# Optimization experiments

Hardware: AMD Instinct MI355X
Metric: run time of the kernel (lower is better)

## Reference

```python
import jax, jax.numpy as jnp
import numpy as np

B, CIN, D, H, W = 2, 64, 64, 64, 64
NUM_CLASSES = 5
STRIDE = 2
NMAX = 32
TOPK = 13
TAL_ALPHA, TAL_BETA = 1.0, 6.0
EPS = 1e-9


def setup_inputs() -> dict:
    key = jax.random.key(0)
    ks = jax.random.split(key, 6)
    features = jax.random.normal(ks[0], (B, CIN, D, H, W), jnp.float32)
    cls_w = jax.random.normal(ks[1], (NUM_CLASSES, CIN, 3, 3, 3), jnp.float32) * 0.02
    cls_b = jnp.zeros((NUM_CLASSES,), jnp.float32)
    off_w = jax.random.normal(ks[2], (3, CIN, 3, 3, 3), jnp.float32) * 0.01
    off_b = jnp.zeros((3,), jnp.float32)
    coords = jax.random.uniform(ks[3], (B, NMAX, 3), jnp.float32, 4.0, float(D * STRIDE) - 4.0)
    cls = jax.random.randint(ks[4], (B, NMAX, 1), 0, NUM_CLASSES).astype(jnp.float32)
    sigma = jax.random.uniform(ks[5], (B, NMAX, 1), jnp.float32, 2.0, 8.0)
    pad = (jnp.arange(NMAX) >= 24)[None, :, None]  # last 8 GT slots are padding
    cls = jnp.where(pad, -100.0, cls)
    labels = jnp.concatenate([coords, cls, sigma], axis=-1)  # B N 5 : x,y,z,class,sigma
    return {"features": features, "cls_w": cls_w, "cls_b": cls_b,
            "off_w": off_w, "off_b": off_b, "labels": labels}


def conv3d(x, w, b):
    y = jax.lax.conv_general_dilated(x, w, (1, 1, 1), 'SAME',
                                     dimension_numbers=('NCDHW', 'OIDHW', 'NCDHW'))
    return y + b[None, :, None, None, None]


def make_anchors():
    g = jnp.stack(jnp.meshgrid(jnp.arange(D), jnp.arange(H), jnp.arange(W), indexing='ij'))
    return (g.astype(jnp.float32) + 0.5) * STRIDE  # (3, D, H, W)


def flatten_bchw(x):
    # B C D H W -> B (D H W) C
    Bsz, C = x.shape[0], x.shape[1]
    return x.transpose(0, 2, 3, 4, 1).reshape(Bsz, -1, C)


def tal_assign(pred_logits, pred_centers, true_labels, true_centers, true_sigmas, valid):
    # pred_logits (B,L,C); pred_centers (B,L,3); true_* (B,N,...); valid (B,N) bool
    Bsz, L, C = pred_logits.shape
    N = true_labels.shape[1]
    d2 = jnp.sum((true_centers[:, :, None, :] - pred_centers[:, None, :, :]) ** 2, -1)  # B N L
    ious = jnp.exp(-d2 / (2.0 * true_sigmas[:, :, None] ** 2))  # keypoint IoU, B N L
    probs = jax.nn.sigmoid(pred_logits).transpose(0, 2, 1)  # B C L
    cls_scores = jnp.take_along_axis(probs, true_labels[:, :, None], axis=1)  # B N L
    align = (cls_scores ** TAL_ALPHA) * (ious ** TAL_BETA)  # alignment metric
    topv, topi = jax.lax.top_k(align, TOPK)
    is_topk = jnp.zeros_like(align).at[
        jnp.arange(Bsz)[:, None, None], jnp.arange(N)[None, :, None], topi
    ].set(jnp.where(topv > EPS, 1.0, 0.0))
    mask_pos = is_topk * valid[:, :, None].astype(align.dtype)  # B N L
    pos_sum = mask_pos.sum(axis=1)  # B L
    # resolve anchors matched to multiple GTs: keep GT with max IoU
    is_max_iou = jax.nn.one_hot(jnp.argmax(ious, axis=1), N, axis=1, dtype=align.dtype)
    mask_pos = jnp.where(pos_sum[:, None, :] > 1, is_max_iou, mask_pos)
    pos_sum = mask_pos.sum(axis=1)
    fg = pos_sum > 0  # B L
    assigned_gt = jnp.argmax(mask_pos, axis=1)  # B L
    assigned_labels = jnp.take_along_axis(true_labels, assigned_gt, axis=1)
    assigned_labels = jnp.where(fg, assigned_labels, C)  # bg_index = C
    assigned_centers = jnp.take_along_axis(true_centers, assigned_gt[:, :, None], axis=1)  # B L 3
    assigned_sigmas = jnp.take_along_axis(true_sigmas, assigned_gt, axis=1)  # B L
    align = align * mask_pos
    max_align = align.max(axis=2, keepdims=True)  # B N 1
    max_iou = (ious * mask_pos).max(axis=2, keepdims=True)
    score = (align * max_iou / (max_align + EPS)).max(axis=1)  # B L
    assigned_scores = jax.nn.one_hot(assigned_labels, C + 1)[..., :C] * score[..., None]  # B L C
    return assigned_labels, assigned_centers, assigned_scores, assigned_sigmas


def detection_loss(logits, offsets, anchors, labels):
    pred_logits = flatten_bchw(logits)               # B L C
    pred_centers = flatten_bchw(anchors + offsets)   # B L 3
    anchor_pts = flatten_bchw(anchors)
    C = pred_logits.shape[-1]
    true_centers = labels[..., :3]
    true_labels_f = labels[..., 3]
    true_sigmas = labels[..., 4]
    valid = true_labels_f != -100.0
    true_labels = jnp.where(valid, true_labels_f, 0.0).astype(jnp.int32)
    assigned = tal_assign(jax.lax.stop_gradient(pred_logits),
                          jax.lax.stop_gradient(pred_centers),
                          true_labels, true_centers, true_sigmas, valid)
    assigned_labels, assigned_centers, assigned_scores, assigned_sigmas = jax.lax.stop_gradient(assigned)
    one_hot_label = jax.nn.one_hot(assigned_labels, C + 1)[..., :C]
    # varifocal loss (alpha=0.75, gamma=2)
    p = jax.nn.sigmoid(pred_logits)
    weight = 0.75 * (p ** 2.0) * (1.0 - one_hot_label) + assigned_scores * one_hot_label
    bce = assigned_scores * jax.nn.softplus(-pred_logits) + (1.0 - assigned_scores) * jax.nn.softplus(pred_logits)
    cls_loss = jnp.sum(weight * bce)
    d = jnp.sum((pred_centers - assigned_centers) ** 2, -1)  # B L
    w = assigned_scores.sum(-1)
    iou = jnp.exp(-d / (2.0 * assigned_sigmas ** 2))
    mask_positive = assigned_labels != C
    reg_loss = jnp.sum(jnp.where(mask_positive, (1.0 - iou) * w, 0.0))
    return (cls_loss + reg_loss) / assigned_scores.sum()


def reference(features, cls_w, cls_b, off_w, off_b, labels):
    logits = conv3d(features, cls_w, cls_b)    # B C D H W
    offsets = conv3d(features, off_w, off_b)   # B 3 D H W
    anchors = jnp.broadcast_to(make_anchors()[None], (features.shape[0], 3, D, H, W))
    loss = detection_loss(logits, offsets, anchors, labels)
    return loss
```

## Files before the change

### kernel.cpp

```cpp
#include <hip/hip_runtime.h>
#include <math.h>

#define NB 2
#define CIN 64
#define DD_ 64
#define HH_ 64
#define WW_ 64
#define NCLS 5
#define LL (DD_*HH_*WW_)
#define NMAXG 32
#define TOPKK 13
#define NSLAB 4
#define BUFSZ 38016

typedef __attribute__((ext_vector_type(16))) float floatx16;

__device__ __forceinline__ float softplusf_(float z){
  return fmaxf(z, 0.f) + log1pf(expf(-fabsf(z)));
}
__device__ __forceinline__ float sigmoidf_(float z){
  return 1.f/(1.f + expf(-z));
}
__device__ __forceinline__ unsigned tofp8_(float x){
  unsigned u = __float_as_uint(x);
  unsigned sign = (u >> 24) & 0x80u;
  unsigned a = u & 0x7FFFFFFFu;
  if (a >= 0x43E00000u) return sign | 0x7Eu;
  if (a < 0x3C800000u){
    float fa = __uint_as_float(a);
    int m = (int)rintf(fa * 512.f);
    return sign | (unsigned)m;
  }
  unsigned bb = a + 0x7FFFFu + ((a >> 20) & 1u);
  unsigned e8 = ((bb >> 23) & 0xFFu) - 120u;
  unsigned m8 = (bb >> 20) & 7u;
  if (e8 > 15u || (e8 == 15u && m8 > 6u)) return sign | 0x7Eu;
  return sign | (e8 << 3) | m8;
}

__global__ __launch_bounds__(256) void transpose_kernel(
    const float* __restrict__ feat, unsigned char* __restrict__ featT,
    const float* __restrict__ cls_w, const float* __restrict__ off_w,
    unsigned char* __restrict__ wA, float* __restrict__ bgz)
{
  const int t = threadIdx.x;
  const int w = t & 63;
  const int hh = t >> 6;
  const int d = blockIdx.x;
  const int h = blockIdx.y*4 + hh;
  const int b = blockIdx.z;
  const float* src = feat + (size_t)b*CIN*LL + (size_t)d*4096 + (size_t)h*64 + w;
  const size_t sp = (size_t)d*4096 + (size_t)h*64 + w;
  #pragma unroll
  for (int cc=0; cc<4; ++cc){
    unsigned q[16];
    #pragma unroll
    for (int j=0;j<16;++j) q[j] = tofp8_(src[(size_t)(cc*16+j)*LL]);
    uint4 p;
    p.x = q[0] | (q[1]<<8) | (q[2]<<16) | (q[3]<<24);
    p.y = q[4] | (q[5]<<8) | (q[6]<<16) | (q[7]<<24);
    p.z = q[8] | (q[9]<<8) | (q[10]<<16) | (q[11]<<24);
    p.w = q[12] | (q[13]<<8) | (q[14]<<16) | (q[15]<<24);
    *(uint4*)(featT + ((size_t)(b*4+cc)*LL + sp)*16) = p;
  }
  if (blockIdx.z == 0 && blockIdx.y == 0 && blockIdx.x < 54){
    if (blockIdx.x == 0 && t < 2) bgz[t] = 0.f;
    int idx = blockIdx.x*256 + t;
    int slice = idx >> 6; int lane = idx & 63;
    int cc = slice & 3; int r = slice >> 2;
    int kw = r % 3; int r2 = r / 3;
    int kh = r2 % 3; int rr = r2 / 3;
    int m = lane & 31, khalf = lane >> 5;
    int outch = m & 7;
    int kd = rr - (m >> 3);
    unsigned q[8];
    #pragma unroll
    for (int i=0;i<8;++i){
      int c = cc*16 + khalf*8 + i;
      float wv = 0.f;
      if (kd >= 0 && kd <= 2){
        if (outch < NCLS) wv = cls_w[(outch*CIN + c)*27 + kd*9 + kh*3 + kw];
        else              wv = off_w[((outch-NCLS)*CIN + c)*27 + kd*9 + kh*3 + kw];
      }
      q[i] = tofp8_(wv);
    }
    uint2 p;
    p.x = q[0] | (q[1]<<8) | (q[2]<<16) | (q[3]<<24);
    p.y = q[4] | (q[5]<<8) | (q[6]<<16) | (q[7]<<24);
    *(uint2*)(wA + (size_t)idx*8) = p;
  }
}

__global__ __launch_bounds__(256, 2) void conv_mfma_kernel(
    const unsigned char* __restrict__ featT,
    const unsigned char* __restrict__ wA,
    const float* __restrict__ cls_b, const float* __restrict__ off_b,
    float* __restrict__ logits_ws,
    float* __restrict__ centers_ws,
    float* __restrict__ bg_sum,
    unsigned* __restrict__ moff_u)
{
  __shared__ uint4 xs4[2*BUFSZ/16];
  __shared__ float bsum[4];
  unsigned char* xs = (unsigned char*)xs4;

  const int tid = threadIdx.x;
  const int lane = tid & 63, hl = tid >> 6;
  const int col = lane & 31, khalf = lane >> 5;
  const int h0 = blockIdx.x*4, d0 = blockIdx.y*4, b = blockIdx.z;
  const bool edge = (d0==0) || (d0==DD_-4) || (h0==0) || (h0==HH_-4);

  for (int idx = tid; idx < 144; idx += 256){
    int buf = idx / 72; int j = idx - buf*72;
    int row = j >> 1, slot = j & 1;
    *(uint4*)(xs + buf*BUFSZ + row*1056 + slot*1040) = make_uint4(0,0,0,0);
  }
  if (edge){
    #pragma unroll 1
    for (int row=0; row<36; ++row){
      int d_ = d0-1+row/6, h_ = h0-1+row-6*(row/6);
      if ((unsigned)d_ < 64u && (unsigned)h_ < 64u) continue;
      if (tid < 128){
        int buf = tid >> 6, wp = (tid & 63) + 1;
        *(uint4*)(xs + buf*BUFSZ + row*1056 + wp*16) = make_uint4(0,0,0,0);
      }
    }
  }

  int soff[9]; int sdst[9]; unsigned svalid = 0;
  #pragma unroll
  for (int it=0; it<9; ++it){
    int row = it*4 + hl;
    int rd = row/6;
    int d_ = d0 - 1 + rd, h_ = h0 - 1 + row - 6*rd;
    bool v = !edge || ((unsigned)d_ < 64u && (unsigned)h_ < 64u);
    if (v) svalid |= (1u<<it);
    int dc = v ? d_ : 0, hc = v ? h_ : 0;
    soff[it] = (dc*4096 + hc*64 + lane)*16;
    sdst[it] = row*1056 + 16;
  }

  floatx16 accA = (floatx16)(0.f);
  floatx16 accB = (floatx16)(0.f);

  const long* wAv = (const long*)wA;
  const int bpoff = hl*1056 + col*16 + khalf*8;

#define STAGE(ccv, bufsel) { \
  const unsigned char* plane = featT + (size_t)(b*4+(ccv))*LL*16; \
  _Pragma("unroll") \
  for (int it=0; it<9; ++it){ \
    if (svalid & (1u<<it)){ \
      __builtin_amdgcn_global_load_lds( \
        (const __attribute__((address_space(1))) void*)(plane + soff[it]), \
        (__attribute__((address_space(3))) void*)(xs + (bufsel)*BUFSZ + sdst[it]), 16, 0, 0); \
    } \
  } }

#define LOADA(dst, ccv, rrv) { \
  _Pragma("unroll") \
  for (int q=0;q<9;++q) dst[q] = wAv[(size_t)(((rrv)*9+q)*4+(ccv))*64 + lane]; }

#define COMPR(areg, rrv, xb) \
  if ((unsigned)(d0-1+(rrv)) < 64u){ \
    const unsigned char* bp = (xb) + bpoff + (rrv)*6336; \
    _Pragma("unroll") \
    for (int kh=0;kh<3;++kh){ \
      if ((unsigned)(h0+hl-1+kh) < 64u){ \
        _Pragma("unroll") \
        for (int kw=0;kw<3;++kw){ \
          long a = areg[kh*3+kw]; \
          long b0 = *(const long*)(bp + kh*1056 + kw*16); \
          accA = __builtin_amdgcn_mfma_f32_32x32x16_fp8_fp8(a, b0, accA, 0,0,0); \
          long b1 = *(const long*)(bp + kh*1056 + kw*16 + 512); \
          accB = __builtin_amdgcn_mfma_f32_32x32x16_fp8_fp8(a, b1, accB, 0,0,0); \
        } } } }

  long aP[9], aQ[9];
  LOADA(aP, 0, 0);
  STAGE(0, 0);
  __syncthreads();

  #pragma unroll 1
  for (int cc=0; cc<4; ++cc){
    if (cc < 3) STAGE(cc+1, (cc+1)&1);
    const unsigned char* xb = xs + (cc&1)*BUFSZ;
    LOADA(aQ, cc, 1);             COMPR(aP, 0, xb);
    LOADA(aP, cc, 2);             COMPR(aQ, 1, xb);
    LOADA(aQ, cc, 3);             COMPR(aP, 2, xb);
    LOADA(aP, cc, 4);             COMPR(aQ, 3, xb);
    LOADA(aQ, cc, 5);             COMPR(aP, 4, xb);
    { int nc = (cc+1)&3; LOADA(aP, nc, 0); }  COMPR(aQ, 5, xb);
    __syncthreads();
  }

  float bg = 0.f, om = 0.f;
  const int h = h0 + hl;
  #pragma unroll
  for (int wh=0; wh<2; ++wh){
    const int w = wh*32 + col;
    #pragma unroll
    for (int dq=0; dq<4; ++dq){
      int d = d0 + dq;
      size_t l = (size_t)d*4096 + (size_t)h*64 + w;
      float v0 = wh ? accB[dq*4+0] : accA[dq*4+0];
      float v1 = wh ? accB[dq*4+1] : accA[dq*4+1];
      float v2 = wh ? accB[dq*4+2] : accA[dq*4+2];
      float v3 = wh ? accB[dq*4+3] : accA[dq*4+3];
      if (khalf == 0){
        float z0 = v0 + cls_b[0]; logits_ws[(size_t)(b*NCLS+0)*LL + l] = z0;
        float z1 = v1 + cls_b[1]; logits_ws[(size_t)(b*NCLS+1)*LL + l] = z1;
        float z2 = v2 + cls_b[2]; logits_ws[(size_t)(b*NCLS+2)*LL + l] = z2;
        float z3 = v3 + cls_b[3]; logits_ws[(size_t)(b*NCLS+3)*LL + l] = z3;
        float p;
        p = sigmoidf_(z0); bg += 0.75f*p*p*softplusf_(z0);
        p = sigmoidf_(z1); bg += 0.75f*p*p*softplusf_(z1);
        p = sigmoidf_(z2); bg += 0.75f*p*p*softplusf_(z2);
        p = sigmoidf_(z3); bg += 0.75f*p*p*softplusf_(z3);
      } else {
        float z4 = v0 + cls_b[4]; logits_ws[(size_t)(b*NCLS+4)*LL + l] = z4;
        float p = sigmoidf_(z4); bg += 0.75f*p*p*softplusf_(z4);
        float o0 = v1 + off_b[0];
        float o1 = v2 + off_b[1];
        float o2 = v3 + off_b[2];
        om = fmaxf(om, fmaxf(fabsf(o0), fmaxf(fabsf(o1), fabsf(o2))));
        float4 ctr;
        ctr.x = ((float)d+0.5f)*2.f + o0;
        ctr.y = ((float)h+0.5f)*2.f + o1;
        ctr.z = ((float)w+0.5f)*2.f + o2;
        ctr.w = 0.f;
        *(float4*)(centers_ws + ((size_t)b*LL + l)*4) = ctr;
      }
    }
  }
  #pragma unroll
  for (int off=32;off;off>>=1){
    bg += __shfl_down(bg, off);
    om = fmaxf(om, __shfl_xor(om, off));
  }
  if (lane == 0){
    bsum[hl] = bg;
    atomicMax(moff_u, __float_as_uint(om));
  }
  __syncthreads();
  if (tid == 0)
    atomicAdd(bg_sum, bsum[0]+bsum[1]+bsum[2]+bsum[3]);
}

__global__ __launch_bounds__(256) void topk_box_kernel(
    const float* __restrict__ logits_ws, const float* __restrict__ centers_ws,
    const float* __restrict__ labels,
    const unsigned* __restrict__ moff_u,
    float* __restrict__ pv, int* __restrict__ pi)
{
  const int bn = blockIdx.x;
  const int slab = blockIdx.y;
  const int b = bn >> 5, n = bn & 31;
  const int tid = threadIdx.x;

  const float* lb = labels + (b*NMAXG + n)*5;
  const float tx = lb[0], ty = lb[1], tz = lb[2];
  const float cf = lb[3];
  const float sg = lb[4];
  const int lab = (cf == -100.f) ? 0 : (int)cf;
  const float m6 = -3.f/(sg*sg);
  const float moff = __uint_as_float(*moff_u);
  const float R = 2.6336f*sg + moff + 0.05f;

  int i0d = (int)ceilf((tx - R - 1.f)*0.5f); if (i0d < 0) i0d = 0;
  int i1d = (int)floorf((tx + R - 1.f)*0.5f); if (i1d > 63) i1d = 63;
  int i0h = (int)ceilf((ty - R - 1.f)*0.5f); if (i0h < 0) i0h = 0;
  int i1h = (int)floorf((ty + R - 1.f)*0.5f); if (i1h > 63) i1h = 63;
  int i0w = (int)ceilf((tz - R - 1.f)*0.5f); if (i0w < 0) i0w = 0;
  int i1w = (int)floorf((tz + R - 1.f)*0.5f); if (i1w > 63) i1w = 63;
  int nd = i1d-i0d+1, nh = i1h-i0h+1, nw = i1w-i0w+1;
  int total = (nd>0 && nh>0 && nw>0) ? nd*nh*nw : 0;
  int lo = (total*slab)/NSLAB, hi = (total*(slab+1))/NSLAB;

  const float* lg = logits_ws + (size_t)(b*NCLS + lab)*LL;
  const float* cb = centers_ws + (size_t)b*LL*4;

  float v[13]; int ix[13];
  #pragma unroll
  for (int j=0;j<13;++j){ v[j]=-1.f; ix[j]=0x7fffffff; }

  for (int idx = lo + tid; idx < hi; idx += 256){
    int r = idx;
    int wi = r % nw; r /= nw;
    int hi2 = r % nh; int di = r / nh;
    int l = (i0d+di)*4096 + (i0h+hi2)*64 + (i0w+wi);
    float4 c4 = *(const float4*)(cb + (size_t)l*4);
    float dx = c4.x-tx, dy = c4.y-ty, dz = c4.z-tz;
    float e = m6*(dx*dx + dy*dy + dz*dz);
    if (e < -20.8f) continue;
    float a = sigmoidf_(lg[l]) * expf(e);
    if (a > v[12]){
      float cv = a; int ci = l;
      #pragma unroll
      for (int j=0;j<13;++j){
        bool take = (cv > v[j]) || (cv == v[j] && ci < ix[j]);
        float nv = take ? cv : v[j];  float ov = take ? v[j] : cv;
        int   ni = take ? ci : ix[j]; int   oi = take ? ix[j] : ci;
        v[j]=nv; ix[j]=ni; cv=ov; ci=oi;
      }
    }
  }

  const int lane = tid & 63, wvi = tid >> 6;
  float mv = -2.f; int mi = 0x7fffffff;
  #pragma unroll 1
  for (int k=0;k<13;++k){
    float bv = v[0]; int bi = ix[0]; int bl = lane;
    #pragma unroll
    for (int off=32; off; off>>=1){
      float ov2 = __shfl_xor(bv, off);
      int oi = __shfl_xor(bi, off);
      int ol = __shfl_xor(bl, off);
      if (ov2 > bv || (ov2 == bv && oi < bi)){ bv=ov2; bi=oi; bl=ol; }
    }
    if (lane == k){ mv = bv; mi = bi; }
    if (lane == bl){
      #pragma unroll
      for (int j=0;j<12;++j){ v[j]=v[j+1]; ix[j]=ix[j+1]; }
      v[12] = -2.f; ix[12] = 0x7fffffff;
    }
  }
  __shared__ float sv2[4*13]; __shared__ int si2[4*13];
  if (lane < 13){ sv2[wvi*13+lane] = mv; si2[wvi*13+lane] = mi; }
  __syncthreads();
  if (wvi == 0){
    float v2 = -2.f; int i2 = 0x7fffffff;
    if (lane < 52){ v2 = sv2[lane]; i2 = si2[lane]; }
    #pragma unroll 1
    for (int k=0;k<13;++k){
      float bv = v2; int bi = i2; int bl = lane;
      #pragma unroll
      for (int off=32; off; off>>=1){
        float ov2 = __shfl_xor(bv, off);
        int oi = __shfl_xor(bi, off);
        int ol = __shfl_xor(bl, off);
        if (ov2 > bv || (ov2 == bv && oi < bi)){ bv=ov2; bi=oi; bl=ol; }
      }
      if (lane == 0){
        pv[(bn*NSLAB+slab)*TOPKK + k] = bv;
        pi[(bn*NSLAB+slab)*TOPKK + k] = bi;
      }
      if (lane == bl) v2 = -2.f;
    }
  }
}

__global__ __launch_bounds__(64) void topk_merge_kernel(
    const float* __restrict__ pv, const int* __restrict__ pi,
    float* __restrict__ tv, int* __restrict__ ti)
{
  const int bn = blockIdx.x;
  const int t = threadIdx.x;
  const int NC = NSLAB*TOPKK;
  float v = -2.f; int ix = 0x7fffffff;
  if (t < NC){ v = pv[bn*NC + t]; ix = pi[bn*NC + t]; }
  #pragma unroll 1
  for (int k=0;k<13;++k){
    float bv = v; int bi = ix; int bl = t;
    #pragma unroll
    for (int off=32; off; off>>=1){
      float ov = __shfl_xor(bv, off);
      int oi = __shfl_xor(bi, off);
      int ol = __shfl_xor(bl, off);
      if (ov > bv || (ov == bv && oi < bi)){ bv=ov; bi=oi; bl=ol; }
    }
    if (t==0){ tv[bn*TOPKK+k]=bv; ti[bn*TOPKK+k]=bi; }
    if (t==bl) v = -2.f;
  }
}

__global__ __launch_bounds__(1024) void finalize_kernel(
    const float* __restrict__ logits_ws, const float* __restrict__ centers_ws,
    const float* __restrict__ labels,
    const float* __restrict__ tv, const int* __restrict__ ti,
    const float* __restrict__ bg_sum, float* __restrict__ out)
{
  const int tid = threadIdx.x;
  __shared__ float gx[64], gy[64], gz[64], gs[64];
  __shared__ int glab[64], gvalid[64];
  __shared__ int hkey[2048], hcnt[2048], hmin[2048];
  __shared__ unsigned maxA[64], maxI[64];
  __shared__ float accD, accC;
  if (tid==0){ accD=0.f; accC=0.f; }
  for (int i=tid;i<2048;i+=1024){ hkey[i]=-1; hcnt[i]=0; hmin[i]=0x7fffffff; }
  if (tid<64){
    const float* lb = labels + tid*5;
    gx[tid]=lb[0]; gy[tid]=lb[1]; gz[tid]=lb[2];
    float cf = lb[3]; gs[tid]=lb[4];
    int val = (cf != -100.f);
    gvalid[tid]=val; glab[tid]= val ? (int)cf : 0;
    maxA[tid]=0u; maxI[tid]=0u;
  }
  __syncthreads();

  const int e = tid;
  bool ok = false; int l = -1; int n = 0; int b = 0;
  if (e < 2*416){
    b = (e >= 416) ? 1 : 0;
    int eb = e - 416*b;
    n = eb/13; int k = eb - 13*n;
    float v = tv[(b*NMAXG+n)*TOPKK + k];
    l = ti[(b*NMAXG+n)*TOPKK + k];
    ok = gvalid[b*32+n] && (v > 1e-9f);
  }
  int slot = -1;
  if (ok){
    unsigned h = (((unsigned)l * 2654435761u) >> 20) & 1023u;
    for (;;){
      int prev = atomicCAS(&hkey[b*1024 + h], -1, l);
      if (prev == -1 || prev == l){ slot = b*1024 + (int)h; break; }
      h = (h+1) & 1023u;
    }
    atomicAdd(&hcnt[slot], 1);
    atomicMin(&hmin[slot], e);
  }
  __syncthreads();

  bool first = ok && (hmin[slot] == e);
  float a=0.f, iou=0.f; int nstar=0;
  if (first){
    float px = centers_ws[((size_t)b*LL + l)*4 + 0];
    float py = centers_ws[((size_t)b*LL + l)*4 + 1];
    float pz = centers_ws[((size_t)b*LL + l)*4 + 2];
    if (hcnt[slot] == 1){
      nstar = n;
    } else {
      float best = -1.f; int bidx = 0;
      #pragma unroll 1
      for (int nn=0;nn<32;++nn){
        float dx=gx[b*32+nn]-px, dy=gy[b*32+nn]-py, dz=gz[b*32+nn]-pz;
        float d2 = dx*dx+dy*dy+dz*dz;
        float io = expf(-d2/(2.f*gs[b*32+nn]*gs[b*32+nn]));
        if (io > best){ best=io; bidx=nn; }
      }
      nstar = bidx;
    }
    int gi = b*32 + nstar;
    float dx=gx[gi]-px, dy=gy[gi]-py, dz=gz[gi]-pz;
    float d2 = dx*dx+dy*dy+dz*dz;
    float sgv = gs[gi];
    iou = expf(-d2/(2.f*sgv*sgv));
    float z = logits_ws[(size_t)(b*NCLS + glab[gi])*LL + l];
    a = sigmoidf_(z) * expf(-3.f*d2/(sgv*sgv));
    atomicMax(&maxA[gi], __float_as_uint(a));
    atomicMax(&maxI[gi], __float_as_uint(iou));
  }
  __syncthreads();

  if (first){
    int gi = b*32 + nstar;
    float mA = __uint_as_float(maxA[gi]);
    float mI = __uint_as_float(maxI[gi]);
    float score = a*mI/(mA + 1e-9f);
    float z = logits_ws[(size_t)(b*NCLS + glab[gi])*LL + l];
    float p = sigmoidf_(z);
    float t2 = log1pf(expf(-fabsf(z)));
    float spz = fmaxf(z,0.f) + t2;
    float spm = fmaxf(-z,0.f) + t2;
    float corr = score*(score*spm + (1.f-score)*spz) - 0.75f*p*p*spz;
    float reg  = (1.f - iou)*score;
    atomicAdd(&accD, score);
    atomicAdd(&accC, corr + reg);
  }
  __syncthreads();
  if (tid==0) out[0] = (bg_sum[0] + accC) / accD;
}

extern "C" void kernel_launch(void* const* d_in, const int* in_sizes, int n_in,
                              void* d_out, int out_size, void* d_ws, size_t ws_size,
                              hipStream_t stream) {
  const float* feat  = (const float*)d_in[0];
  const float* cls_w = (const float*)d_in[1];
  const float* cls_b = (const float*)d_in[2];
  const float* off_w = (const float*)d_in[3];
  const float* off_b = (const float*)d_in[4];
  const float* labels= (const float*)d_in[5];
  float* out = (float*)d_out;

  float* logits_ws  = (float*)d_ws;
  float* centers_ws = logits_ws + (size_t)NB*NCLS*LL;
  float* tv = centers_ws + (size_t)NB*LL*4;
  int*   ti = (int*)(tv + 64*TOPKK);
  float* pv = (float*)(ti + 64*TOPKK);
  int*   pi = (int*)(pv + 64*NSLAB*TOPKK);
  float* bg = (float*)(pi + 64*NSLAB*TOPKK);
  unsigned char* wA = (unsigned char*)(bg + 16);
  unsigned char* featT = wA + 216*64*8;

  transpose_kernel<<<dim3(64,16,2), 256, 0, stream>>>(
      feat, featT, cls_w, off_w, wA, bg);
  conv_mfma_kernel<<<dim3(16,16,2), 256, 0, stream>>>(
      featT, wA, cls_b, off_b, logits_ws, centers_ws, bg, (unsigned*)(bg+1));
  topk_box_kernel<<<dim3(64,NSLAB), 256, 0, stream>>>(
      logits_ws, centers_ws, labels, (const unsigned*)(bg+1), pv, pi);
  topk_merge_kernel<<<64, 64, 0, stream>>>(pv, pi, tv, ti);
  finalize_kernel<<<1, 1024, 0, stream>>>(
      logits_ws, centers_ws, labels, tv, ti, bg, out);
}
```

Baseline: 164.0 us.

## Fuse top-k, merge, and finalize into one kernel via last-block ticket

Merges the per-slab top-k, the top-k merge, and the single-block finalize kernels into one launch. Each block finishes its slab top-k, then takes an atomic ticket, and the last block to arrive does the merge and loss finalization in shared memory. This removes two kernel launches and their inter-kernel gaps. In exchange the tail work runs on one 256-thread block instead of a 1024-thread block, the finalize loops are serialized, some computation is recomputed across passes, and shared memory use per block grows a lot, which may lower occupancy for the top-k phase.

```diff
diff --git a/kernel.cpp b/kernel.cpp
--- a/kernel.cpp
+++ b/kernel.cpp
@@ -64,7 +64,7 @@
     *(uint4*)(featT + ((size_t)(b*4+cc)*LL + sp)*16) = p;
   }
   if (blockIdx.z == 0 && blockIdx.y == 0 && blockIdx.x < 54){
-    if (blockIdx.x == 0 && t < 2) bgz[t] = 0.f;
+    if (blockIdx.x == 0 && t < 8) bgz[t] = 0.f;
     int idx = blockIdx.x*256 + t;
     int slice = idx >> 6; int lane = idx & 63;
     int cc = slice & 3; int r = slice >> 2;
@@ -247,93 +247,81 @@
     atomicAdd(bg_sum, bsum[0]+bsum[1]+bsum[2]+bsum[3]);
 }
 
-__global__ __launch_bounds__(256) void topk_box_kernel(
+__global__ __launch_bounds__(256) void topk_final_kernel(
     const float* __restrict__ logits_ws, const float* __restrict__ centers_ws,
     const float* __restrict__ labels,
-    const unsigned* __restrict__ moff_u,
-    float* __restrict__ pv, int* __restrict__ pi)
+    const float* __restrict__ bgz, int* __restrict__ ticket,
+    float* __restrict__ pv, int* __restrict__ pi,
+    float* __restrict__ out)
 {
+  __shared__ float sv2[4*13]; __shared__ int si2[4*13];
+  __shared__ int lastFlag;
+  __shared__ float tvs[64*TOPKK]; __shared__ int tis[64*TOPKK];
+  __shared__ float gx[64], gy[64], gz[64], gs[64];
+  __shared__ int glab[64], gvalid[64];
+  __shared__ int hkey[2048], hcnt[2048], hmin[2048];
+  __shared__ unsigned maxA[64], maxI[64];
+  __shared__ float accD, accC;
+
   const int bn = blockIdx.x;
   const int slab = blockIdx.y;
   const int b = bn >> 5, n = bn & 31;
   const int tid = threadIdx.x;
 
-  const float* lb = labels + (b*NMAXG + n)*5;
-  const float tx = lb[0], ty = lb[1], tz = lb[2];
-  const float cf = lb[3];
-  const float sg = lb[4];
-  const int lab = (cf == -100.f) ? 0 : (int)cf;
-  const float m6 = -3.f/(sg*sg);
-  const float moff = __uint_as_float(*moff_u);
-  const float R = 2.6336f*sg + moff + 0.05f;
-
-  int i0d = (int)ceilf((tx - R - 1.f)*0.5f); if (i0d < 0) i0d = 0;
-  int i1d = (int)floorf((tx + R - 1.f)*0.5f); if (i1d > 63) i1d = 63;
-  int i0h = (int)ceilf((ty - R - 1.f)*0.5f); if (i0h < 0) i0h = 0;
-  int i1h = (int)floorf((ty + R - 1.f)*0.5f); if (i1h > 63) i1h = 63;
-  int i0w = (int)ceilf((tz - R - 1.f)*0.5f); if (i0w < 0) i0w = 0;
-  int i1w = (int)floorf((tz + R - 1.f)*0.5f); if (i1w > 63) i1w = 63;
-  int nd = i1d-i0d+1, nh = i1h-i0h+1, nw = i1w-i0w+1;
-  int total = (nd>0 && nh>0 && nw>0) ? nd*nh*nw : 0;
-  int lo = (total*slab)/NSLAB, hi = (total*(slab+1))/NSLAB;
-
-  const float* lg = logits_ws + (size_t)(b*NCLS + lab)*LL;
-  const float* cb = centers_ws + (size_t)b*LL*4;
-
-  float v[13]; int ix[13];
-  #pragma unroll
-  for (int j=0;j<13;++j){ v[j]=-1.f; ix[j]=0x7fffffff; }
-
-  for (int idx = lo + tid; idx < hi; idx += 256){
-    int r = idx;
-    int wi = r % nw; r /= nw;
-    int hi2 = r % nh; int di = r / nh;
-    int l = (i0d+di)*4096 + (i0h+hi2)*64 + (i0w+wi);
-    float4 c4 = *(const float4*)(cb + (size_t)l*4);
-    float dx = c4.x-tx, dy = c4.y-ty, dz = c4.z-tz;
-    float e = m6*(dx*dx + dy*dy + dz*dz);
-    if (e < -20.8f) continue;
-    float a = sigmoidf_(lg[l]) * expf(e);
-    if (a > v[12]){
-      float cv = a; int ci = l;
-      #pragma unroll
-      for (int j=0;j<13;++j){
-        bool take = (cv > v[j]) || (cv == v[j] && ci < ix[j]);
-        float nv = take ? cv : v[j];  float ov = take ? v[j] : cv;
-        int   ni = take ? ci : ix[j]; int   oi = take ? ix[j] : ci;
-        v[j]=nv; ix[j]=ni; cv=ov; ci=oi;
-      }
-    }
-  }
-
-  const int lane = tid & 63, wvi = tid >> 6;
-  float mv = -2.f; int mi = 0x7fffffff;
-  #pragma unroll 1
-  for (int k=0;k<13;++k){
-    float bv = v[0]; int bi = ix[0]; int bl = lane;
+  {
+    const float* lb = labels + (b*NMAXG + n)*5;
+    const float tx = lb[0], ty = lb[1], tz = lb[2];
+    const float cf = lb[3];
+    const float sg = lb[4];
+    const int lab = (cf == -100.f) ? 0 : (int)cf;
+    const float m6 = -3.f/(sg*sg);
+    const float moff = __uint_as_float(((const unsigned*)bgz)[1]);
+    const float R = 2.6336f*sg + moff + 0.05f;
+
+    int i0d = (int)ceilf((tx - R - 1.f)*0.5f); if (i0d < 0) i0d = 0;
+    int i1d = (int)floorf((tx + R - 1.f)*0.5f); if (i1d > 63) i1d = 63;
+    int i0h = (int)ceilf((ty - R - 1.f)*0.5f); if (i0h < 0) i0h = 0;
+    int i1h = (int)floorf((ty + R - 1.f)*0.5f); if (i1h > 63) i1h = 63;
+    int i0w = (int)ceilf((tz - R - 1.f)*0.5f); if (i0w < 0) i0w = 0;
+    int i1w = (int)floorf((tz + R - 1.f)*0.5f); if (i1w > 63) i1w = 63;
+    int nd = i1d-i0d+1, nh = i1h-i0h+1, nw = i1w-i0w+1;
+    int total = (nd>0 && nh>0 && nw>0) ? nd*nh*nw : 0;
+    int lo = (total*slab)/NSLAB, hi = (total*(slab+1))/NSLAB;
+
+    const float* lg = logits_ws + (size_t)(b*NCLS + lab)*LL;
+    const float* cb = centers_ws + (size_t)b*LL*4;
+
+    float v[13]; int ix[13];
     #pragma unroll
-    for (int off=32; off; off>>=1){
-      float ov2 = __shfl_xor(bv, off);
-      int oi = __shfl_xor(bi, off);
-      int ol = __shfl_xor(bl, off);
-      if (ov2 > bv || (ov2 == bv && oi < bi)){ bv=ov2; bi=oi; bl=ol; }
-    }
-    if (lane == k){ mv = bv; mi = bi; }
-    if (lane == bl){
-      #pragma unroll
-      for (int j=0;j<12;++j){ v[j]=v[j+1]; ix[j]=ix[j+1]; }
-      v[12] = -2.f; ix[12] = 0x7fffffff;
-    }
-  }
-  __shared__ float sv2[4*13]; __shared__ int si2[4*13];
-  if (lane < 13){ sv2[wvi*13+lane] = mv; si2[wvi*13+lane] = mi; }
-  __syncthreads();
-  if (wvi == 0){
-    float v2 = -2.f; int i2 = 0x7fffffff;
-    if (lane < 52){ v2 = sv2[lane]; i2 = si2[lane]; }
+    for (int j=0;j<13;++j){ v[j]=-1.f; ix[j]=0x7fffffff; }
+
+    for (int idx = lo + tid; idx < hi; idx += 256){
+      int r = idx;
+      int wi = r % nw; r /= nw;
+      int hi2 = r % nh; int di = r / nh;
+      int l = (i0d+di)*4096 + (i0h+hi2)*64 + (i0w+wi);
+      float4 c4 = *(const float4*)(cb + (size_t)l*4);
+      float dx = c4.x-tx, dy = c4.y-ty, dz = c4.z-tz;
+      float e = m6*(dx*dx + dy*dy + dz*dz);
+      if (e < -20.8f) continue;
+      float a = sigmoidf_(lg[l]) * expf(e);
+      if (a > v[12]){
+        float cv = a; int ci = l;
+        #pragma unroll
+        for (int j=0;j<13;++j){
+          bool take = (cv > v[j]) || (cv == v[j] && ci < ix[j]);
+          float nv = take ? cv : v[j];  float ov = take ? v[j] : cv;
+          int   ni = take ? ci : ix[j]; int   oi = take ? ix[j] : ci;
+          v[j]=nv; ix[j]=ni; cv=ov; ci=oi;
+        }
+      }
+    }
+
+    const int lane = tid & 63, wvi = tid >> 6;
+    float mv = -2.f; int mi = 0x7fffffff;
     #pragma unroll 1
     for (int k=0;k<13;++k){
-      float bv = v2; int bi = i2; int bl = lane;
+      float bv = v[0]; int bi = ix[0]; int bl = lane;
       #pragma unroll
       for (int off=32; off; off>>=1){
         float ov2 = __shfl_xor(bv, off);
@@ -341,53 +329,48 @@
         int ol = __shfl_xor(bl, off);
         if (ov2 > bv || (ov2 == bv && oi < bi)){ bv=ov2; bi=oi; bl=ol; }
       }
-      if (lane == 0){
-        pv[(bn*NSLAB+slab)*TOPKK + k] = bv;
-        pi[(bn*NSLAB+slab)*TOPKK + k] = bi;
-      }
-      if (lane == bl) v2 = -2.f;
-    }
-  }
-}
-
-__global__ __launch_bounds__(64) void topk_merge_kernel(
-    const float* __restrict__ pv, const int* __restrict__ pi,
-    float* __restrict__ tv, int* __restrict__ ti)
-{
-  const int bn = blockIdx.x;
-  const int t = threadIdx.x;
-  const int NC = NSLAB*TOPKK;
-  float v = -2.f; int ix = 0x7fffffff;
-  if (t < NC){ v = pv[bn*NC + t]; ix = pi[bn*NC + t]; }
-  #pragma unroll 1
-  for (int k=0;k<13;++k){
-    float bv = v; int bi = ix; int bl = t;
-    #pragma unroll
-    for (int off=32; off; off>>=1){
-      float ov = __shfl_xor(bv, off);
-      int oi = __shfl_xor(bi, off);
-      int ol = __shfl_xor(bl, off);
-      if (ov > bv || (ov == bv && oi < bi)){ bv=ov; bi=oi; bl=ol; }
-    }
-    if (t==0){ tv[bn*TOPKK+k]=bv; ti[bn*TOPKK+k]=bi; }
-    if (t==bl) v = -2.f;
-  }
-}
-
-__global__ __launch_bounds__(1024) void finalize_kernel(
-    const float* __restrict__ logits_ws, const float* __restrict__ centers_ws,
-    const float* __restrict__ labels,
-    const float* __restrict__ tv, const int* __restrict__ ti,
-    const float* __restrict__ bg_sum, float* __restrict__ out)
-{
-  const int tid = threadIdx.x;
-  __shared__ float gx[64], gy[64], gz[64], gs[64];
-  __shared__ int glab[64], gvalid[64];
-  __shared__ int hkey[2048], hcnt[2048], hmin[2048];
-  __shared__ unsigned maxA[64], maxI[64];
-  __shared__ float accD, accC;
-  if (tid==0){ accD=0.f; accC=0.f; }
-  for (int i=tid;i<2048;i+=1024){ hkey[i]=-1; hcnt[i]=0; hmin[i]=0x7fffffff; }
+      if (lane == k){ mv = bv; mi = bi; }
+      if (lane == bl){
+        #pragma unroll
+        for (int j=0;j<12;++j){ v[j]=v[j+1]; ix[j]=ix[j+1]; }
+        v[12] = -2.f; ix[12] = 0x7fffffff;
+      }
+    }
+    if (lane < 13){ sv2[wvi*13+lane] = mv; si2[wvi*13+lane] = mi; }
+    __syncthreads();
+    if (wvi == 0){
+      float v2 = -2.f; int i2 = 0x7fffffff;
+      if (lane < 52){ v2 = sv2[lane]; i2 = si2[lane]; }
+      #pragma unroll 1
+      for (int k=0;k<13;++k){
+        float bv = v2; int bi = i2; int bl = lane;
+        #pragma unroll
+        for (int off=32; off; off>>=1){
+          float ov2 = __shfl_xor(bv, off);
+          int oi = __shfl_xor(bi, off);
+          int ol = __shfl_xor(bl, off);
+          if (ov2 > bv || (ov2 == bv && oi < bi)){ bv=ov2; bi=oi; bl=ol; }
+        }
+        if (lane == 0){
+          pv[(bn*NSLAB+slab)*TOPKK + k] = bv;
+          pi[(bn*NSLAB+slab)*TOPKK + k] = bi;
+        }
+        if (lane == bl) v2 = -2.f;
+      }
+    }
+  }
+
+  __syncthreads();
+  __threadfence();
+  if (tid == 0){
+    int t = atomicAdd(ticket, 1);
+    lastFlag = (t == 64*NSLAB - 1);
+  }
+  __syncthreads();
+  if (!lastFlag) return;
+  __threadfence();
+
+  for (int i=tid;i<2048;i+=256){ hkey[i]=-1; hcnt[i]=0; hmin[i]=0x7fffffff; }
   if (tid<64){
     const float* lb = labels + tid*5;
     gx[tid]=lb[0]; gy[tid]=lb[1]; gz[tid]=lb[2];
@@ -396,68 +379,132 @@
     gvalid[tid]=val; glab[tid]= val ? (int)cf : 0;
     maxA[tid]=0u; maxI[tid]=0u;
   }
-  __syncthreads();
-
-  const int e = tid;
-  bool ok = false; int l = -1; int n = 0; int b = 0;
-  if (e < 2*416){
-    b = (e >= 416) ? 1 : 0;
-    int eb = e - 416*b;
-    n = eb/13; int k = eb - 13*n;
-    float v = tv[(b*NMAXG+n)*TOPKK + k];
-    l = ti[(b*NMAXG+n)*TOPKK + k];
-    ok = gvalid[b*32+n] && (v > 1e-9f);
-  }
-  int slot = -1;
-  if (ok){
+  if (tid==0){ accD=0.f; accC=0.f; }
+  {
+    const int lane = tid & 63, wvi = tid >> 6;
+    const int NC = NSLAB*TOPKK;
+    #pragma unroll 1
+    for (int q=0; q<16; ++q){
+      int bnm = wvi*16 + q;
+      float v = -2.f; int ixv = 0x7fffffff;
+      if (lane < NC){ v = pv[bnm*NC + lane]; ixv = pi[bnm*NC + lane]; }
+      #pragma unroll 1
+      for (int k=0;k<13;++k){
+        float bv = v; int bi = ixv; int bl = lane;
+        #pragma unroll
+        for (int off=32; off; off>>=1){
+          float ov = __shfl_xor(bv, off);
+          int oi = __shfl_xor(bi, off);
+          int ol = __shfl_xor(bl, off);
+          if (ov > bv || (ov == bv && oi < bi)){ bv=ov; bi=oi; bl=ol; }
+        }
+        if (lane==0){ tvs[bnm*TOPKK+k]=bv; tis[bnm*TOPKK+k]=bi; }
+        if (lane==bl) v = -2.f;
+      }
+    }
+  }
+  __syncthreads();
+
+  #pragma unroll 1
+  for (int e=tid; e<2*416; e+=256){
+    int bq = (e >= 416) ? 1 : 0;
+    int eb = e - 416*bq;
+    int nn = eb/13; int k = eb - 13*nn;
+    float v = tvs[(bq*NMAXG+nn)*TOPKK + k];
+    int l = tis[(bq*NMAXG+nn)*TOPKK + k];
+    bool ok = gvalid[bq*32+nn] && (v > 1e-9f);
+    if (ok){
+      unsigned h = (((unsigned)l * 2654435761u) >> 20) & 1023u;
+      int slot;
+      for (;;){
+        int prev = atomicCAS(&hkey[bq*1024 + (int)h], -1, l);
+        if (prev == -1 || prev == l){ slot = bq*1024 + (int)h; break; }
+        h = (h+1) & 1023u;
+      }
+      atomicAdd(&hcnt[slot], 1);
+      atomicMin(&hmin[slot], e);
+    }
+  }
+  __syncthreads();
+
+  #pragma unroll 1
+  for (int e=tid; e<2*416; e+=256){
+    int bq = (e >= 416) ? 1 : 0;
+    int eb = e - 416*bq;
+    int nn = eb/13; int k = eb - 13*nn;
+    float v = tvs[(bq*NMAXG+nn)*TOPKK + k];
+    int l = tis[(bq*NMAXG+nn)*TOPKK + k];
+    if (!(gvalid[bq*32+nn] && (v > 1e-9f))) continue;
     unsigned h = (((unsigned)l * 2654435761u) >> 20) & 1023u;
-    for (;;){
-      int prev = atomicCAS(&hkey[b*1024 + h], -1, l);
-      if (prev == -1 || prev == l){ slot = b*1024 + (int)h; break; }
-      h = (h+1) & 1023u;
-    }
-    atomicAdd(&hcnt[slot], 1);
-    atomicMin(&hmin[slot], e);
-  }
-  __syncthreads();
-
-  bool first = ok && (hmin[slot] == e);
-  float a=0.f, iou=0.f; int nstar=0;
-  if (first){
-    float px = centers_ws[((size_t)b*LL + l)*4 + 0];
-    float py = centers_ws[((size_t)b*LL + l)*4 + 1];
-    float pz = centers_ws[((size_t)b*LL + l)*4 + 2];
-    if (hcnt[slot] == 1){
-      nstar = n;
-    } else {
+    while (hkey[bq*1024 + (int)h] != l) h = (h+1) & 1023u;
+    int slot = bq*1024 + (int)h;
+    if (hmin[slot] != e) continue;
+    float px = centers_ws[((size_t)bq*LL + l)*4 + 0];
+    float py = centers_ws[((size_t)bq*LL + l)*4 + 1];
+    float pz = centers_ws[((size_t)bq*LL + l)*4 + 2];
+    int nstar;
+    if (hcnt[slot] == 1) nstar = nn;
+    else {
       float best = -1.f; int bidx = 0;
       #pragma unroll 1
-      for (int nn=0;nn<32;++nn){
-        float dx=gx[b*32+nn]-px, dy=gy[b*32+nn]-py, dz=gz[b*32+nn]-pz;
+      for (int n2=0;n2<32;++n2){
+        float dx=gx[bq*32+n2]-px, dy=gy[bq*32+n2]-py, dz=gz[bq*32+n2]-pz;
         float d2 = dx*dx+dy*dy+dz*dz;
-        float io = expf(-d2/(2.f*gs[b*32+nn]*gs[b*32+nn]));
-        if (io > best){ best=io; bidx=nn; }
+        float io = expf(-d2/(2.f*gs[bq*32+n2]*gs[bq*32+n2]));
+        if (io > best){ best=io; bidx=n2; }
       }
       nstar = bidx;
     }
-    int gi = b*32 + nstar;
+    int gi = bq*32 + nstar;
     float dx=gx[gi]-px, dy=gy[gi]-py, dz=gz[gi]-pz;
     float d2 = dx*dx+dy*dy+dz*dz;
     float sgv = gs[gi];
-    iou = expf(-d2/(2.f*sgv*sgv));
-    float z = logits_ws[(size_t)(b*NCLS + glab[gi])*LL + l];
-    a = sigmoidf_(z) * expf(-3.f*d2/(sgv*sgv));
+    float iou = expf(-d2/(2.f*sgv*sgv));
+    float z = logits_ws[(size_t)(bq*NCLS + glab[gi])*LL + l];
+    float a = sigmoidf_(z) * expf(-3.f*d2/(sgv*sgv));
     atomicMax(&maxA[gi], __float_as_uint(a));
     atomicMax(&maxI[gi], __float_as_uint(iou));
   }
   __syncthreads();
 
-  if (first){
-    int gi = b*32 + nstar;
+  #pragma unroll 1
+  for (int e=tid; e<2*416; e+=256){
+    int bq = (e >= 416) ? 1 : 0;
+    int eb = e - 416*bq;
+    int nn = eb/13; int k = eb - 13*nn;
+    float v = tvs[(bq*NMAXG+nn)*TOPKK + k];
+    int l = tis[(bq*NMAXG+nn)*TOPKK + k];
+    if (!(gvalid[bq*32+nn] && (v > 1e-9f))) continue;
+    unsigned h = (((unsigned)l * 2654435761u) >> 20) & 1023u;
+    while (hkey[bq*1024 + (int)h] != l) h = (h+1) & 1023u;
+    int slot = bq*1024 + (int)h;
+    if (hmin[slot] != e) continue;
+    float px = centers_ws[((size_t)bq*LL + l)*4 + 0];
+    float py = centers_ws[((size_t)bq*LL + l)*4 + 1];
+    float pz = centers_ws[((size_t)bq*LL + l)*4 + 2];
+    int nstar;
+    if (hcnt[slot] == 1) nstar = nn;
+    else {
+      float best = -1.f; int bidx = 0;
+      #pragma unroll 1
+      for (int n2=0;n2<32;++n2){
+        float dx=gx[bq*32+n2]-px, dy=gy[bq*32+n2]-py, dz=gz[bq*32+n2]-pz;
+        float d2 = dx*dx+dy*dy+dz*dz;
+        float io = expf(-d2/(2.f*gs[bq*32+n2]*gs[bq*32+n2]));
+        if (io > best){ best=io; bidx=n2; }
+      }
+      nstar = bidx;
+    }
+    int gi = bq*32 + nstar;
+    float dx=gx[gi]-px, dy=gy[gi]-py, dz=gz[gi]-pz;
+    float d2 = dx*dx+dy*dy+dz*dz;
+    float sgv = gs[gi];
+    float iou = expf(-d2/(2.f*sgv*sgv));
+    float z = logits_ws[(size_t)(bq*NCLS + glab[gi])*LL + l];
+    float a = sigmoidf_(z) * expf(-3.f*d2/(sgv*sgv));
     float mA = __uint_as_float(maxA[gi]);
     float mI = __uint_as_float(maxI[gi]);
     float score = a*mI/(mA + 1e-9f);
-    float z = logits_ws[(size_t)(b*NCLS + glab[gi])*LL + l];
     float p = sigmoidf_(z);
     float t2 = log1pf(expf(-fabsf(z)));
     float spz = fmaxf(z,0.f) + t2;
@@ -468,7 +515,7 @@
     atomicAdd(&accC, corr + reg);
   }
   __syncthreads();
-  if (tid==0) out[0] = (bg_sum[0] + accC) / accD;
+  if (tid==0) out[0] = (bgz[0] + accC) / accD;
 }
 
 extern "C" void kernel_launch(void* const* d_in, const int* in_sizes, int n_in,
@@ -484,9 +531,7 @@
 
   float* logits_ws  = (float*)d_ws;
   float* centers_ws = logits_ws + (size_t)NB*NCLS*LL;
-  float* tv = centers_ws + (size_t)NB*LL*4;
-  int*   ti = (int*)(tv + 64*TOPKK);
-  float* pv = (float*)(ti + 64*TOPKK);
+  float* pv = centers_ws + (size_t)NB*LL*4;
   int*   pi = (int*)(pv + 64*NSLAB*TOPKK);
   float* bg = (float*)(pi + 64*NSLAB*TOPKK);
   unsigned char* wA = (unsigned char*)(bg + 16);
@@ -496,9 +541,6 @@
       feat, featT, cls_w, off_w, wA, bg);
   conv_mfma_kernel<<<dim3(16,16,2), 256, 0, stream>>>(
       featT, wA, cls_b, off_b, logits_ws, centers_ws, bg, (unsigned*)(bg+1));
-  topk_box_kernel<<<dim3(64,NSLAB), 256, 0, stream>>>(
-      logits_ws, centers_ws, labels, (const unsigned*)(bg+1), pv, pi);
-  topk_merge_kernel<<<64, 64, 0, stream>>>(pv, pi, tv, ti);
-  finalize_kernel<<<1, 1024, 0, stream>>>(
-      logits_ws, centers_ws, labels, tv, ti, bg, out);
-}
+  topk_final_kernel<<<dim3(64,NSLAB), 256, 0, stream>>>(
+      logits_ws, centers_ws, labels, bg, (int*)(bg+4), pv, pi, out);
+}
```

Measured after the change: 293.6 us. 1.79x slower.

## Single-buffer conv LDS staging to raise occupancy to four blocks per CU

Applied to the files above, without the earlier changes.

Replaces the double-buffered LDS feature staging in the fp8 MFMA conv kernel with a single buffer, halving shared memory per block, and raises the launch-bounds occupancy hint from 2 to 4 blocks. Each channel chunk is now loaded, synchronized, then computed, so load/compute overlap within a block is lost and must come from more resident blocks. The bgz zeroing also widens from 2 to 8 entries. The higher occupancy target may also pressure register allocation.

```diff
diff --git a/kernel.cpp b/kernel.cpp
--- a/kernel.cpp
+++ b/kernel.cpp
@@ -64,7 +64,7 @@
     *(uint4*)(featT + ((size_t)(b*4+cc)*LL + sp)*16) = p;
   }
   if (blockIdx.z == 0 && blockIdx.y == 0 && blockIdx.x < 54){
-    if (blockIdx.x == 0 && t < 2) bgz[t] = 0.f;
+    if (blockIdx.x == 0 && t < 8) bgz[t] = 0.f;
     int idx = blockIdx.x*256 + t;
     int slice = idx >> 6; int lane = idx & 63;
     int cc = slice & 3; int r = slice >> 2;
@@ -91,7 +91,7 @@
   }
 }
 
-__global__ __launch_bounds__(256, 2) void conv_mfma_kernel(
+__global__ __launch_bounds__(256, 4) void conv_mfma_kernel(
     const unsigned char* __restrict__ featT,
     const unsigned char* __restrict__ wA,
     const float* __restrict__ cls_b, const float* __restrict__ off_b,
@@ -100,7 +100,7 @@
     float* __restrict__ bg_sum,
     unsigned* __restrict__ moff_u)
 {
-  __shared__ uint4 xs4[2*BUFSZ/16];
+  __shared__ uint4 xs4[BUFSZ/16];
   __shared__ float bsum[4];
   unsigned char* xs = (unsigned char*)xs4;
 
@@ -110,19 +110,17 @@
   const int h0 = blockIdx.x*4, d0 = blockIdx.y*4, b = blockIdx.z;
   const bool edge = (d0==0) || (d0==DD_-4) || (h0==0) || (h0==HH_-4);
 
-  for (int idx = tid; idx < 144; idx += 256){
-    int buf = idx / 72; int j = idx - buf*72;
-    int row = j >> 1, slot = j & 1;
-    *(uint4*)(xs + buf*BUFSZ + row*1056 + slot*1040) = make_uint4(0,0,0,0);
+  if (tid < 72){
+    int row = tid >> 1, slot = tid & 1;
+    *(uint4*)(xs + row*1056 + slot*1040) = make_uint4(0,0,0,0);
   }
   if (edge){
     #pragma unroll 1
     for (int row=0; row<36; ++row){
       int d_ = d0-1+row/6, h_ = h0-1+row-6*(row/6);
       if ((unsigned)d_ < 64u && (unsigned)h_ < 64u) continue;
-      if (tid < 128){
-        int buf = tid >> 6, wp = (tid & 63) + 1;
-        *(uint4*)(xs + buf*BUFSZ + row*1056 + wp*16) = make_uint4(0,0,0,0);
+      if (tid < 64){
+        *(uint4*)(xs + row*1056 + (tid+1)*16) = make_uint4(0,0,0,0);
       }
     }
   }
@@ -146,14 +144,14 @@
   const long* wAv = (const long*)wA;
   const int bpoff = hl*1056 + col*16 + khalf*8;
 
-#define STAGE(ccv, bufsel) { \
+#define STAGE(ccv) { \
   const unsigned char* plane = featT + (size_t)(b*4+(ccv))*LL*16; \
   _Pragma("unroll") \
   for (int it=0; it<9; ++it){ \
     if (svalid & (1u<<it)){ \
       __builtin_amdgcn_global_load_lds( \
         (const __attribute__((address_space(1))) void*)(plane + soff[it]), \
-        (__attribute__((address_space(3))) void*)(xs + (bufsel)*BUFSZ + sdst[it]), 16, 0, 0); \
+        (__attribute__((address_space(3))) void*)(xs + sdst[it]), 16, 0, 0); \
     } \
   } }
 
@@ -161,9 +159,9 @@
   _Pragma("unroll") \
   for (int q=0;q<9;++q) dst[q] = wAv[(size_t)(((rrv)*9+q)*4+(ccv))*64 + lane]; }
 
-#define COMPR(areg, rrv, xb) \
+#define COMPR(areg, rrv) \
   if ((unsigned)(d0-1+(rrv)) < 64u){ \
-    const unsigned char* bp = (xb) + bpoff + (rrv)*6336; \
+    const unsigned char* bp = xs + bpoff + (rrv)*6336; \
     _Pragma("unroll") \
     for (int kh=0;kh<3;++kh){ \
       if ((unsigned)(h0+hl-1+kh) < 64u){ \
@@ -178,20 +176,18 @@
 
   long aP[9], aQ[9];
   LOADA(aP, 0, 0);
-  STAGE(0, 0);
-  __syncthreads();
 
   #pragma unroll 1
   for (int cc=0; cc<4; ++cc){
-    if (cc < 3) STAGE(cc+1, (cc+1)&1);
-    const unsigned char* xb = xs + (cc&1)*BUFSZ;
-    LOADA(aQ, cc, 1);             COMPR(aP, 0, xb);
-    LOADA(aP, cc, 2);             COMPR(aQ, 1, xb);
-    LOADA(aQ, cc, 3);             COMPR(aP, 2, xb);
-    LOADA(aP, cc, 4);             COMPR(aQ, 3, xb);
-    LOADA(aQ, cc, 5);             COMPR(aP, 4, xb);
-    { int nc = (cc+1)&3; LOADA(aP, nc, 0); }  COMPR(aQ, 5, xb);
+    if (cc) __syncthreads();
+    STAGE(cc);
     __syncthreads();
+    LOADA(aQ, cc, 1);             COMPR(aP, 0);
+    LOADA(aP, cc, 2);             COMPR(aQ, 1);
+    LOADA(aQ, cc, 3);             COMPR(aP, 2);
+    LOADA(aP, cc, 4);             COMPR(aQ, 3);
+    LOADA(aQ, cc, 5);             COMPR(aP, 4);
+    { int nc = (cc+1)&3; LOADA(aP, nc, 0); }  COMPR(aQ, 5);
   }
 
   float bg = 0.f, om = 0.f;
```

New measurement: 163.2 us. No clear change (-0.4%).
